# Optimization experiments

Measured on AMD Instinct MI355X. Metric: run time of the kernel, lower is better.

Reference implementation:

```python
import jax, jax.numpy as jnp
import numpy as np

N = 200_000
E = 6_400_000
EPS = 1e-12


def l2_normalize(x):
    # F.normalize(x, p=2, dim=1): x / max(||x||_2, eps)
    n = jnp.linalg.norm(x, axis=1, keepdims=True)
    return x / jnp.maximum(n, EPS)


def gcn_conv(x, W, b, src, dst, n):
    """PyG GCNConv: add self-loops, symmetric normalization D^-1/2 A D^-1/2,
    linear transform (no bias) on nodes, scatter-add to targets, then + bias."""
    loop = jnp.arange(n)
    s = jnp.concatenate([src, loop])  # sources (messages gathered here)
    d = jnp.concatenate([dst, loop])  # targets (aggregation here)
    deg = jax.ops.segment_sum(jnp.ones(s.shape[0], dtype=x.dtype), d, num_segments=n)
    dinv = jnp.where(deg > 0, jax.lax.rsqrt(deg), 0.0)
    norm = dinv[s] * dinv[d]  # [E+N]
    h = x @ W  # [N, out]
    out = jax.ops.segment_sum(norm[:, None] * h[s], d, num_segments=n)
    return out + b


def setup_inputs() -> dict:
    key = jax.random.key(0)
    ks = jax.random.split(key, 10)
    x = jax.random.normal(ks[0], (N, 3), dtype=jnp.float32)
    edge_index = jax.random.randint(ks[1], (2, E), 0, N, dtype=jnp.int64)

    def glorot(k, shape):
        lim = float(np.sqrt(6.0 / (shape[0] + shape[1])))
        return jax.random.uniform(k, shape, jnp.float32, -lim, lim)

    return {
        "x": x,
        "edge_index": edge_index,
        "W1": glorot(ks[2], (3, 6)),   "b1": jnp.zeros((6,), jnp.float32),
        "W2": glorot(ks[3], (6, 12)),  "b2": jnp.zeros((12,), jnp.float32),
        "W3": glorot(ks[4], (12, 24)), "b3": jnp.zeros((24,), jnp.float32),
        "Wc": glorot(ks[5], (24, 13)), "bc": jnp.zeros((13,), jnp.float32),
    }


def reference(x, edge_index, W1, b1, W2, b2, W3, b3, Wc, bc):
    src, dst = edge_index[0], edge_index[1]
    n = x.shape[0]
    h = jnp.tanh(gcn_conv(x, W1, b1, src, dst, n))
    h = jnp.tanh(l2_normalize(gcn_conv(h, W2, b2, src, dst, n)))
    h = l2_normalize(gcn_conv(h, W3, b3, src, dst, n))
    h = h @ Wc + bc
    return l2_normalize(h)
```

## Files before the change

kernel.cpp:

```cpp
#include <hip/hip_runtime.h>
#include <math.h>


static constexpr int NN = 200000;
static constexpr int NE = 6400000;
static constexpr int BK = 256;

static constexpr int SUBW  = 512;
static constexpr int NBA   = (NN + SUBW - 1) / SUBW;
static constexpr int QDS   = 128;
static constexpr int BKB   = 512;
static constexpr int NBB   = ((NBA + 7) / 8) * 8 * 4;
static constexpr int LCAP  = 4864;
static constexpr int NBL   = 1024;
static constexpr int BKC   = 512;
static constexpr int SEG   = (NE + NBL - 1) / NBL;
static constexpr int SRCSH = 13;
static constexpr int NSB   = (NN + (1 << SRCSH) - 1) >> SRCSH;

static constexpr int S     = 4;
static constexpr int LOGS  = 2;

__global__ void __launch_bounds__(BKC) k_count(const int* __restrict__ dstI,
                                               int* __restrict__ hist, int e) {
  __shared__ int cnt[NBA];
  for (int t = threadIdx.x; t < NBA; t += BKC) cnt[t] = 0;
  __syncthreads();
  int blk = blockIdx.x;
  int st = blk * SEG, en = st + SEG; if (en > e) en = e;
  int i = st + (int)threadIdx.x;
  for (; i + 3 * BKC < en; i += 4 * BKC) {
    int d0 = __builtin_nontemporal_load(dstI + i);
    int d1 = __builtin_nontemporal_load(dstI + i + BKC);
    int d2 = __builtin_nontemporal_load(dstI + i + 2 * BKC);
    int d3 = __builtin_nontemporal_load(dstI + i + 3 * BKC);
    atomicAdd(&cnt[d0 >> 9], 1);
    atomicAdd(&cnt[d1 >> 9], 1);
    atomicAdd(&cnt[d2 >> 9], 1);
    atomicAdd(&cnt[d3 >> 9], 1);
  }
  for (; i < en; i += BKC) {
    int d = __builtin_nontemporal_load(dstI + i);
    atomicAdd(&cnt[d >> 9], 1);
  }
  __syncthreads();
  for (int t = threadIdx.x; t < NBA; t += BKC) hist[(size_t)t * NBL + blk] = cnt[t];
}

__global__ void __launch_bounds__(256) k_scanrow(int* __restrict__ hist,
                                                 int* __restrict__ tot) {
  __shared__ int s0[256], s1[256];
  int b = blockIdx.x, t = threadIdx.x;
  int* row = hist + (size_t)b * NBL;
  uint4 vv = ((const uint4*)row)[t];
  int v0 = (int)vv.x, v1 = (int)vv.y, v2 = (int)vv.z, v3 = (int)vv.w;
  int s = v0 + v1 + v2 + v3;
  s0[t] = s;
  __syncthreads();
  int* a = s0; int* bb = s1;
  for (int o = 1; o < 256; o <<= 1) {
    bb[t] = a[t] + ((t >= o) ? a[t - o] : 0);
    __syncthreads();
    int* tmp = a; a = bb; bb = tmp;
  }
  int ex = a[t] - s;
  uint4 w;
  w.x = (unsigned)ex;
  w.y = (unsigned)(ex + v0);
  w.z = (unsigned)(ex + v0 + v1);
  w.w = (unsigned)(ex + v0 + v1 + v2);
  ((uint4*)row)[t] = w;
  if (t == 255) tot[b] = a[t];
}

__global__ void k_scanbin(const int* __restrict__ tot, int* __restrict__ sbase) {
  __shared__ int s0[512], s1[512];
  int t = threadIdx.x;
  int v = (t < NBA) ? tot[t] : 0;
  s0[t] = v;
  __syncthreads();
  int* a = s0; int* b = s1;
  for (int o = 1; o < 512; o <<= 1) {
    b[t] = a[t] + ((t >= o) ? a[t - o] : 0);
    __syncthreads();
    int* tmp = a; a = b; b = tmp;
  }
  if (t < NBA) sbase[t] = a[t] - v;
  if (t == NBA - 1) sbase[NBA] = a[t];
}

__global__ void __launch_bounds__(BKC) k_scat(const int* __restrict__ srcI,
                                              const int* __restrict__ dstI,
                                              const int* __restrict__ hist,
                                              const int* __restrict__ tot,
                                              const int* __restrict__ sbase,
                                              unsigned* __restrict__ stg, int e) {
  __shared__ int pref[NBA];
  __shared__ int cur[NBA];
  __shared__ unsigned lstg[SEG];
  __shared__ int s0[BKC], s1[BKC];
  int blk = blockIdx.x;
  int t = threadIdx.x;
  int h0 = 0, lc = 0;
  if (t < NBA) {
    h0 = hist[(size_t)t * NBL + blk];
    int h1 = (blk < NBL - 1) ? hist[(size_t)t * NBL + blk + 1] : tot[t];
    lc = h1 - h0;
  }
  s0[t] = lc;
  __syncthreads();
  int* a = s0; int* b = s1;
  for (int o = 1; o < BKC; o <<= 1) {
    b[t] = a[t] + ((t >= o) ? a[t - o] : 0);
    __syncthreads();
    int* tmp = a; a = b; b = tmp;
  }
  if (t < NBA) {
    int ex = a[t] - lc;
    pref[t] = ex;
    cur[t] = ex;
  }
  __syncthreads();
  int st = blk * SEG, en = st + SEG; if (en > e) en = e;
  int i = st + t;
  for (; i + 3 * BKC < en; i += 4 * BKC) {
    int s0v = __builtin_nontemporal_load(srcI + i);
    int d0 = __builtin_nontemporal_load(dstI + i);
    int s1v = __builtin_nontemporal_load(srcI + i + BKC);
    int d1 = __builtin_nontemporal_load(dstI + i + BKC);
    int s2v = __builtin_nontemporal_load(srcI + i + 2 * BKC);
    int d2 = __builtin_nontemporal_load(dstI + i + 2 * BKC);
    int s3v = __builtin_nontemporal_load(srcI + i + 3 * BKC);
    int d3 = __builtin_nontemporal_load(dstI + i + 3 * BKC);
    int p0 = atomicAdd(&cur[d0 >> 9], 1);
    int p1 = atomicAdd(&cur[d1 >> 9], 1);
    int p2 = atomicAdd(&cur[d2 >> 9], 1);
    int p3 = atomicAdd(&cur[d3 >> 9], 1);
    lstg[p0] = ((unsigned)(d0 & (SUBW - 1)) << 18) | (unsigned)s0v;
    lstg[p1] = ((unsigned)(d1 & (SUBW - 1)) << 18) | (unsigned)s1v;
    lstg[p2] = ((unsigned)(d2 & (SUBW - 1)) << 18) | (unsigned)s2v;
    lstg[p3] = ((unsigned)(d3 & (SUBW - 1)) << 18) | (unsigned)s3v;
  }
  for (; i < en; i += BKC) {
    int sv = __builtin_nontemporal_load(srcI + i);
    int d = __builtin_nontemporal_load(dstI + i);
    int p = atomicAdd(&cur[d >> 9], 1);
    lstg[p] = ((unsigned)(d & (SUBW - 1)) << 18) | (unsigned)sv;
  }
  __syncthreads();
  if (t < NBA && lc > 0) {
    int lo = pref[t];
    int g = sbase[t] + h0;
    for (int j = 0; j < lc; ++j) stg[g + j] = lstg[lo + j];
  }
}

__global__ void __launch_bounds__(BKB) k_build(const unsigned* __restrict__ stg,
                                               const int* __restrict__ sbase,
                                               int* __restrict__ rowptr,
                                               int* __restrict__ adj,
                                               int* __restrict__ b8,
                                               int* __restrict__ b13,
                                               int* __restrict__ b17) {
  __shared__ unsigned hist2[QDS * NSB];
  __shared__ int htot[QDS];
  __shared__ int s0[QDS], s1[QDS];
  __shared__ unsigned astg[LCAP];
  __shared__ int beforeCnt;
  int g = blockIdx.x;
  int x = g & 7, j = g >> 3;
  int q = j & 3;
  int bin = (j >> 2) * 8 + x;
  if (bin >= NBA) return;
  int base = sbase[bin];
  int m = sbase[bin + 1] - base;
  size_t off = (size_t)base;
  if (g == 0 && threadIdx.x == 0) rowptr[NN] = sbase[NBA];
  for (int t = threadIdx.x; t < QDS * NSB; t += BKB) hist2[t] = 0;
  if (threadIdx.x == 0) beforeCnt = 0;
  __syncthreads();
  int myBefore = 0;
  for (int k = threadIdx.x; k < m; k += BKB) {
    unsigned rec = stg[off + k];
    int dl = (int)(rec >> 18);
    int dq = dl >> 7;
    if (dq == q) {
      int sb = (int)((rec & 0x3FFFFu) >> SRCSH);
      atomicAdd(&hist2[(dl & (QDS - 1)) * NSB + sb], 1u);
    } else if (dq < q) {
      ++myBefore;
    }
  }
  if (myBefore) atomicAdd(&beforeCnt, myBefore);
  __syncthreads();
  if (threadIdx.x < QDS) {
    int dl = threadIdx.x;
    unsigned run = 0;
    for (int sb = 0; sb < NSB; ++sb) {
      unsigned c = hist2[dl * NSB + sb];
      hist2[dl * NSB + sb] = run;
      run += c;
    }
    htot[dl] = (int)run;
    s0[dl] = (int)run;
  }
  __syncthreads();
  int* a = s0; int* bb = s1;
  for (int o2 = 1; o2 < QDS; o2 <<= 1) {
    if (threadIdx.x < QDS) {
      int t = threadIdx.x;
      bb[t] = a[t] + ((t >= o2) ? a[t - o2] : 0);
    }
    __syncthreads();
    int* tmp = a; a = bb; bb = tmp;
  }
  int mytot = a[QDS - 1];
  int base_eff = base + beforeCnt;
  if (threadIdx.x < QDS) {
    int t = threadIdx.x;
    int node = bin * SUBW + q * QDS + t;
    int ex = a[t] - htot[t];
    if (node < NN) {
      rowptr[node] = base_eff + ex;
      b8[node]  = base_eff + ex + (int)hist2[t * NSB + 8];
      b13[node] = base_eff + ex + (int)hist2[t * NSB + 13];
      b17[node] = base_eff + ex + (int)hist2[t * NSB + 17];
    }
    bb[t] = ex;
  }
  __syncthreads();
  for (int k = threadIdx.x; k < m; k += BKB) {
    unsigned rec = stg[off + k];
    int dl = (int)(rec >> 18);
    if ((dl >> 7) != q) continue;
    unsigned src = rec & 0x3FFFFu;
    int sb = (int)(src >> SRCSH);
    int p = bb[dl & (QDS - 1)] + (int)atomicAdd(&hist2[(dl & (QDS - 1)) * NSB + sb], 1u);
    if (p < LCAP) astg[p] = src;
    else adj[base_eff + p] = (int)src;
  }
  __syncthreads();
  int mm = mytot < LCAP ? mytot : LCAP;
  for (int k = threadIdx.x; k < mm; k += BKB) adj[base_eff + k] = (int)astg[k];
}

__global__ void k_prep(const float* __restrict__ x, const int* __restrict__ rowptr,
                       float* __restrict__ dinv, float* __restrict__ p1, int n) {
  int i = blockIdx.x * blockDim.x + threadIdx.x;
  if (i >= n) return;
  float di = rsqrtf(1.0f + (float)(rowptr[i + 1] - rowptr[i]));
  dinv[i] = di;
  float3 v;
  v.x = di * x[3 * (size_t)i];
  v.y = di * x[3 * (size_t)i + 1];
  v.z = di * x[3 * (size_t)i + 2];
  *(float3*)(p1 + 3 * (size_t)i) = v;
}

template <int RW> struct RowT;
template <> struct RowT<3> {
  using T = float3;
  static __device__ inline T ld(const float* __restrict__ p) { return *(const float3*)p; }
  static __device__ inline void add(float* __restrict__ a, const T& v) {
    a[0] += v.x; a[1] += v.y; a[2] += v.z;
  }
  static __device__ inline void st(float* __restrict__ p, const float* __restrict__ a) {
    *(float3*)p = make_float3(a[0], a[1], a[2]);
  }
};
template <> struct RowT<6> {
  struct T { float2 a, b, c; };
  static __device__ inline T ld(const float* __restrict__ p) {
    T t; t.a = *(const float2*)p; t.b = *(const float2*)(p + 2); t.c = *(const float2*)(p + 4);
    return t;
  }
  static __device__ inline void add(float* __restrict__ a, const T& v) {
    a[0] += v.a.x; a[1] += v.a.y; a[2] += v.b.x; a[3] += v.b.y; a[4] += v.c.x; a[5] += v.c.y;
  }
  static __device__ inline void st(float* __restrict__ p, const float* __restrict__ a) {
    *(float2*)(p)     = make_float2(a[0], a[1]);
    *(float2*)(p + 2) = make_float2(a[2], a[3]);
    *(float2*)(p + 4) = make_float2(a[4], a[5]);
  }
};
template <> struct RowT<12> {
  struct T { float4 a, b, c; };
  static __device__ inline T ld(const float* __restrict__ p) {
    T t; t.a = *(const float4*)p; t.b = *(const float4*)(p + 4); t.c = *(const float4*)(p + 8);
    return t;
  }
  static __device__ inline void add(float* __restrict__ a, const T& v) {
    a[0] += v.a.x; a[1] += v.a.y; a[2] += v.a.z; a[3] += v.a.w;
    a[4] += v.b.x; a[5] += v.b.y; a[6] += v.b.z; a[7] += v.b.w;
    a[8] += v.c.x; a[9] += v.c.y; a[10] += v.c.z; a[11] += v.c.w;
  }
  static __device__ inline void st(float* __restrict__ p, const float* __restrict__ a) {
    *(float4*)(p)     = make_float4(a[0], a[1], a[2], a[3]);
    *(float4*)(p + 4) = make_float4(a[4], a[5], a[6], a[7]);
    *(float4*)(p + 8) = make_float4(a[8], a[9], a[10], a[11]);
  }
};

template <int RW, int UN>
__device__ inline void gather_p(const int* __restrict__ adj, int st, int en,
                                const float* __restrict__ pin, float* __restrict__ acc,
                                int slot) {
  using RT = RowT<RW>;
  using T = typename RT::T;
  int k = st + slot;
  if (k + (UN - 1) * S < en) {
    int a[UN];
#pragma unroll
    for (int u = 0; u < UN; ++u) a[u] = adj[k + u * S];
    for (;;) {
      int kn = k + UN * S;
      bool more = (kn + (UN - 1) * S < en);
      int b[UN];
#pragma unroll
      for (int u = 0; u < UN; ++u) b[u] = 0;
      if (more) {
#pragma unroll
        for (int u = 0; u < UN; ++u) b[u] = adj[kn + u * S];
      }
      T v[UN];
#pragma unroll
      for (int u = 0; u < UN; ++u) v[u] = RT::ld(pin + (size_t)a[u] * RW);
#pragma unroll
      for (int u = 0; u < UN; ++u) RT::add(acc, v[u]);
      k = kn;
      if (!more) break;
#pragma unroll
      for (int u = 0; u < UN; ++u) a[u] = b[u];
    }
  }
  for (; k < en; k += S) {
    T v = RT::ld(pin + (size_t)adj[k] * RW);
    RT::add(acc, v);
  }
}

template <int FIN>
__device__ inline void group_reduce(float* __restrict__ acc) {
#pragma unroll
  for (int j = 0; j < FIN; ++j) {
    acc[j] += __shfl_xor(acc[j], 1);
    acc[j] += __shfl_xor(acc[j], 2);
  }
}

template <int RW, int FOUT, int MODE>
__global__ void __launch_bounds__(BK, 8) k_gather_fused(
    const int* __restrict__ adj, const int* __restrict__ rowptr,
    const float* __restrict__ pin, const float* __restrict__ W,
    const float* __restrict__ bias, const float* __restrict__ dinv,
    float* __restrict__ pout, int n) {
  __shared__ float sW[RW * FOUT];
  __shared__ float sb[FOUT];
  for (int t = threadIdx.x; t < RW * FOUT; t += BK) sW[t] = W[t];
  if (threadIdx.x < FOUT) sb[threadIdx.x] = bias[threadIdx.x];
  __syncthreads();
  int g = blockIdx.x * blockDim.x + threadIdx.x;
  int i = g >> LOGS;
  int slot = g & (S - 1);
  if (i >= n) return;
  float acc[RW] = {};
  if (slot == 0) {
    typename RowT<RW>::T v = RowT<RW>::ld(pin + (size_t)i * RW);
    RowT<RW>::add(acc, v);
  }
  gather_p<RW, 4>(adj, rowptr[i], rowptr[i + 1], pin, acc, slot);
  group_reduce<RW>(acc);
  float di = dinv[i];
  float h[FOUT];
  float ss = 0.f;
#pragma unroll
  for (int j = 0; j < FOUT; ++j) {
    float s = 0.f;
#pragma unroll
    for (int kk = 0; kk < RW; ++kk) s = fmaf(acc[kk], sW[kk * FOUT + j], s);
    float t = fmaf(di, s, sb[j]);
    h[j] = t;
    ss += t * t;
  }
  float o[FOUT];
  if (MODE == 0) {
#pragma unroll
    for (int j = 0; j < FOUT; ++j) o[j] = di * tanhf(h[j]);
  } else {
    float inv = 1.f / fmaxf(sqrtf(ss), 1e-12f);
#pragma unroll
    for (int j = 0; j < FOUT; ++j) o[j] = di * tanhf(h[j] * inv);
  }
  if (slot == 0) {
    float* po = pout + (size_t)i * FOUT;
    if (MODE == 0) {
      *(float2*)(po)     = make_float2(o[0], o[1]);
      *(float2*)(po + 2) = make_float2(o[2], o[3]);
      *(float2*)(po + 4) = make_float2(o[4], o[5]);
    } else {
      *(float4*)(po)     = make_float4(o[0], o[1], o[2], o[3]);
      *(float4*)(po + 4) = make_float4(o[4], o[5], o[6], o[7]);
      *(float4*)(po + 8) = make_float4(o[8], o[9], o[10], o[11]);
    }
  }
}

template <int RW, bool FIRST>
__global__ void __launch_bounds__(BK, 8) k_gphase(
    const int* __restrict__ adj, const int* __restrict__ stA,
    const int* __restrict__ enB, const float* __restrict__ pin,
    float* __restrict__ accb, int n) {
  int g = blockIdx.x * blockDim.x + threadIdx.x;
  int i = g >> LOGS;
  int slot = g & (S - 1);
  if (i >= n) return;
  float acc[RW] = {};
  if (slot == 0) {
    if (FIRST) {
      typename RowT<RW>::T v = RowT<RW>::ld(pin + (size_t)i * RW);
      RowT<RW>::add(acc, v);
    } else {
      typename RowT<RW>::T v = RowT<RW>::ld(accb + (size_t)i * RW);
      RowT<RW>::add(acc, v);
    }
  }
  gather_p<RW, 4>(adj, stA[i], enB[i], pin, acc, slot);
  group_reduce<RW>(acc);
  if (slot == 0) RowT<RW>::st(accb + (size_t)i * RW, acc);
}

template <int RW, int FOUT, int MODE>
__global__ void __launch_bounds__(BK, 6) k_gphase_last(
    const int* __restrict__ adj, const int* __restrict__ stA,
    const int* __restrict__ rowptr, const float* __restrict__ pin,
    const float* __restrict__ W, const float* __restrict__ bias,
    const float* __restrict__ Wc, const float* __restrict__ bc,
    const float* __restrict__ dinv, const float* __restrict__ accb,
    float* __restrict__ out, int n) {
  constexpr int FC = 13;
  __shared__ float sW[RW * FOUT];
  __shared__ float sb[FOUT];
  __shared__ float sWc[MODE == 2 ? FOUT * FC : 1];
  __shared__ float sbc[MODE == 2 ? FC : 1];
  for (int t = threadIdx.x; t < RW * FOUT; t += BK) sW[t] = W[t];
  if (threadIdx.x < FOUT) sb[threadIdx.x] = bias[threadIdx.x];
  if (MODE == 2) {
    for (int t = threadIdx.x; t < FOUT * FC; t += BK) sWc[t] = Wc[t];
    if (threadIdx.x < FC) sbc[threadIdx.x] = bc[threadIdx.x];
  }
  __syncthreads();
  int g = blockIdx.x * blockDim.x + threadIdx.x;
  int i = g >> LOGS;
  int slot = g & (S - 1);
  if (i >= n) return;
  float acc[RW] = {};
  if (slot == 0) {
    typename RowT<RW>::T v = RowT<RW>::ld(accb + (size_t)i * RW);
    RowT<RW>::add(acc, v);
  }
  gather_p<RW, 4>(adj, stA[i], rowptr[i + 1], pin, acc, slot);
  group_reduce<RW>(acc);
  float di = dinv[i];
  float h[FOUT];
  float ss = 0.f;
#pragma unroll
  for (int j = 0; j < FOUT; ++j) {
    float s = 0.f;
#pragma unroll
    for (int kk = 0; kk < RW; ++kk) s = fmaf(acc[kk], sW[kk * FOUT + j], s);
    float t = fmaf(di, s, sb[j]);
    h[j] = t;
    ss += t * t;
  }
  float inv = 1.f / fmaxf(sqrtf(ss), 1e-12f);
  if (MODE == 1) {
    float o[FOUT];
#pragma unroll
    for (int j = 0; j < FOUT; ++j) o[j] = di * tanhf(h[j] * inv);
    if (slot == 0) {
      float* po = out + (size_t)i * FOUT;
      *(float4*)(po)     = make_float4(o[0], o[1], o[2], o[3]);
      *(float4*)(po + 4) = make_float4(o[4], o[5], o[6], o[7]);
      *(float4*)(po + 8) = make_float4(o[8], o[9], o[10], o[11]);
    }
  } else {
    float v[FC];
    float ss2 = 0.f;
#pragma unroll
    for (int j = 0; j < FC; ++j) {
      float s = sbc[j];
#pragma unroll
      for (int kk = 0; kk < FOUT; ++kk) s = fmaf(h[kk] * inv, sWc[kk * FC + j], s);
      v[j] = s;
      ss2 += s * s;
    }
    float inv2 = 1.f / fmaxf(sqrtf(ss2), 1e-12f);
    if (slot == 0) {
#pragma unroll
      for (int j = 0; j < FC; ++j) out[(size_t)i * FC + j] = v[j] * inv2;
    }
  }
}

extern "C" void kernel_launch(void* const* d_in, const int* in_sizes, int n_in,
                              void* d_out, int out_size, void* d_ws, size_t ws_size,
                              hipStream_t stream) {
  const float* x  = (const float*)d_in[0];
  const int*   ei = (const int*)d_in[1];
  const float* W1 = (const float*)d_in[2];
  const float* b1 = (const float*)d_in[3];
  const float* W2 = (const float*)d_in[4];
  const float* b2 = (const float*)d_in[5];
  const float* W3 = (const float*)d_in[6];
  const float* b3 = (const float*)d_in[7];
  const float* Wc = (const float*)d_in[8];
  const float* bc = (const float*)d_in[9];
  float* out = (float*)d_out;

  const int n = NN;
  const int e = NE;
  const int* srcI = ei;
  const int* dstI = ei + e;

  float* ws = (float*)d_ws;
  float* dinv  = ws;
  int* rowptr  = (int*)(ws + n);
  int* sbase   = rowptr + n + 8;
  int* tot     = sbase + 512;
  int* hist    = tot + 512;
  int* adj     = hist + NBA * NBL;
  int* b8      = adj + e;
  int* b13     = b8 + n;
  int* b17     = b13 + n;
  size_t roff = (size_t)n + (n + 8) + 512 + 512 + (size_t)NBA * NBL + e + 3 * (size_t)n;
  roff = (roff + 15) & ~(size_t)15;
  float* R     = ws + roff;
  unsigned* stg = (unsigned*)R;
  float* p1   = R;
  float* p2   = R + (size_t)3 * n;
  float* p3   = R + (size_t)9 * n;
  float* accb = R + (size_t)21 * n;

  const int gn  = (n + BK - 1) / BK;
  const int gnS = (n * S + BK - 1) / BK;

  k_count<<<NBL, BKC, 0, stream>>>(dstI, hist, e);
  k_scanrow<<<NBA, 256, 0, stream>>>(hist, tot);
  k_scanbin<<<1, 512, 0, stream>>>(tot, sbase);
  k_scat<<<NBL, BKC, 0, stream>>>(srcI, dstI, hist, tot, sbase, stg, e);
  k_build<<<NBB, BKB, 0, stream>>>(stg, sbase, rowptr, adj, b8, b13, b17);

  k_prep<<<gn, BK, 0, stream>>>(x, rowptr, dinv, p1, n);

  k_gather_fused<3, 6, 0><<<gnS, BK, 0, stream>>>(adj, rowptr, p1, W1, b1, dinv, p2, n);

  k_gphase<6, true><<<gnS, BK, 0, stream>>>(adj, rowptr, b13, p2, accb, n);
  k_gphase_last<6, 12, 1><<<gnS, BK, 0, stream>>>(adj, b13, rowptr, p2, W2, b2,
                                                  Wc, bc, dinv, accb, p3, n);

  k_gphase<12, true><<<gnS, BK, 0, stream>>>(adj, rowptr, b8, p3, accb, n);
  k_gphase<12, false><<<gnS, BK, 0, stream>>>(adj, b8, b17, p3, accb, n);
  k_gphase_last<12, 24, 2><<<gnS, BK, 0, stream>>>(adj, b17, rowptr, p3, W3, b3,
                                                   Wc, bc, dinv, accb, out, n);
}
```

Measured before the change: 389.3 us.

## Split CSR build bins into halves with 4 source ranges instead of fine histograms

The adjacency build kernel now handles half of each 512-node destination bin per block (2 blocks per bin instead of 4). It also replaces the 25-bucket source histogram per destination with 4 coarse source ranges, whose boundaries line up with the old bucket indices 8, 13 and 17. This halves the redundant rescans of each bin's staged records and shrinks the shared-memory histogram and its serial prefix loop, making room for a larger local staging buffer. In exchange, each block does more work, fewer blocks are launched, and edges inside a source range are no longer sorted as finely, which may hurt locality in later gathers.

```diff
diff --git a/kernel.cpp b/kernel.cpp
--- a/kernel.cpp
+++ b/kernel.cpp
@@ -8,15 +8,16 @@
 
 static constexpr int SUBW  = 512;
 static constexpr int NBA   = (NN + SUBW - 1) / SUBW;
-static constexpr int QDS   = 128;
+static constexpr int HDS   = 256;
 static constexpr int BKB   = 512;
-static constexpr int NBB   = ((NBA + 7) / 8) * 8 * 4;
-static constexpr int LCAP  = 4864;
+static constexpr int NBB   = ((NBA + 7) / 8) * 8 * 2;
+static constexpr int LCAP  = 8832;
 static constexpr int NBL   = 1024;
 static constexpr int BKC   = 512;
 static constexpr int SEG   = (NE + NBL - 1) / NBL;
-static constexpr int SRCSH = 13;
-static constexpr int NSB   = (NN + (1 << SRCSH) - 1) >> SRCSH;
+static constexpr int T1    = 65536;
+static constexpr int T2    = 106496;
+static constexpr int T3    = 139264;
 
 static constexpr int S     = 4;
 static constexpr int LOGS  = 2;
@@ -162,43 +163,44 @@
                                                int* __restrict__ b8,
                                                int* __restrict__ b13,
                                                int* __restrict__ b17) {
-  __shared__ unsigned hist2[QDS * NSB];
-  __shared__ int htot[QDS];
-  __shared__ int s0[QDS], s1[QDS];
+  __shared__ unsigned hist2[HDS * 5];
+  __shared__ int htot[HDS];
+  __shared__ int s0[HDS], s1[HDS];
   __shared__ unsigned astg[LCAP];
   __shared__ int beforeCnt;
   int g = blockIdx.x;
   int x = g & 7, j = g >> 3;
-  int q = j & 3;
-  int bin = (j >> 2) * 8 + x;
+  int h = j & 1;
+  int bin = (j >> 1) * 8 + x;
   if (bin >= NBA) return;
   int base = sbase[bin];
   int m = sbase[bin + 1] - base;
   size_t off = (size_t)base;
   if (g == 0 && threadIdx.x == 0) rowptr[NN] = sbase[NBA];
-  for (int t = threadIdx.x; t < QDS * NSB; t += BKB) hist2[t] = 0;
+  for (int t = threadIdx.x; t < HDS * 5; t += BKB) hist2[t] = 0;
   if (threadIdx.x == 0) beforeCnt = 0;
   __syncthreads();
   int myBefore = 0;
   for (int k = threadIdx.x; k < m; k += BKB) {
     unsigned rec = stg[off + k];
     int dl = (int)(rec >> 18);
-    int dq = dl >> 7;
-    if (dq == q) {
-      int sb = (int)((rec & 0x3FFFFu) >> SRCSH);
-      atomicAdd(&hist2[(dl & (QDS - 1)) * NSB + sb], 1u);
-    } else if (dq < q) {
+    if ((dl >> 8) == h) {
+      int src = (int)(rec & 0x3FFFFu);
+      int r = (src >= T1) + (src >= T2) + (src >= T3);
+      atomicAdd(&hist2[(dl & (HDS - 1)) * 5 + r], 1u);
+    } else if (h == 1) {
       ++myBefore;
     }
   }
   if (myBefore) atomicAdd(&beforeCnt, myBefore);
   __syncthreads();
-  if (threadIdx.x < QDS) {
+  if (threadIdx.x < HDS) {
     int dl = threadIdx.x;
     unsigned run = 0;
-    for (int sb = 0; sb < NSB; ++sb) {
-      unsigned c = hist2[dl * NSB + sb];
-      hist2[dl * NSB + sb] = run;
+#pragma unroll
+    for (int r = 0; r < 4; ++r) {
+      unsigned c = hist2[dl * 5 + r];
+      hist2[dl * 5 + r] = run;
       run += c;
     }
     htot[dl] = (int)run;
@@ -206,25 +208,25 @@
   }
   __syncthreads();
   int* a = s0; int* bb = s1;
-  for (int o2 = 1; o2 < QDS; o2 <<= 1) {
-    if (threadIdx.x < QDS) {
+  for (int o2 = 1; o2 < HDS; o2 <<= 1) {
+    if (threadIdx.x < HDS) {
       int t = threadIdx.x;
       bb[t] = a[t] + ((t >= o2) ? a[t - o2] : 0);
     }
     __syncthreads();
     int* tmp = a; a = bb; bb = tmp;
   }
-  int mytot = a[QDS - 1];
+  int mytot = a[HDS - 1];
   int base_eff = base + beforeCnt;
-  if (threadIdx.x < QDS) {
+  if (threadIdx.x < HDS) {
     int t = threadIdx.x;
-    int node = bin * SUBW + q * QDS + t;
+    int node = bin * SUBW + h * HDS + t;
     int ex = a[t] - htot[t];
     if (node < NN) {
       rowptr[node] = base_eff + ex;
-      b8[node]  = base_eff + ex + (int)hist2[t * NSB + 8];
-      b13[node] = base_eff + ex + (int)hist2[t * NSB + 13];
-      b17[node] = base_eff + ex + (int)hist2[t * NSB + 17];
+      b8[node]  = base_eff + ex + (int)hist2[t * 5 + 1];
+      b13[node] = base_eff + ex + (int)hist2[t * 5 + 2];
+      b17[node] = base_eff + ex + (int)hist2[t * 5 + 3];
     }
     bb[t] = ex;
   }
@@ -232,12 +234,12 @@
   for (int k = threadIdx.x; k < m; k += BKB) {
     unsigned rec = stg[off + k];
     int dl = (int)(rec >> 18);
-    if ((dl >> 7) != q) continue;
-    unsigned src = rec & 0x3FFFFu;
-    int sb = (int)(src >> SRCSH);
-    int p = bb[dl & (QDS - 1)] + (int)atomicAdd(&hist2[(dl & (QDS - 1)) * NSB + sb], 1u);
-    if (p < LCAP) astg[p] = src;
-    else adj[base_eff + p] = (int)src;
+    if ((dl >> 8) != h) continue;
+    int src = (int)(rec & 0x3FFFFu);
+    int r = (src >= T1) + (src >= T2) + (src >= T3);
+    int p = bb[dl & (HDS - 1)] + (int)atomicAdd(&hist2[(dl & (HDS - 1)) * 5 + r], 1u);
+    if (p < LCAP) astg[p] = (unsigned)src;
+    else adj[base_eff + p] = src;
   }
   __syncthreads();
   int mm = mytot < LCAP ? mytot : LCAP;
```

Measured after the change: 388.1 us (median of 2 runs). No clear change (-0.3%).
